# Kernel tuning notes

Measured on AMD Instinct MI355X. Metric: run time of the kernel, lower is better.

The kernel has to match this reference:

```python
import jax, jax.numpy as jnp
import numpy as np

WINDOW = 21
PATCH = 1
H_PARAM = 0.1
EPS = 1e-10


def _box_sum(x, w):
    # Sum over a w x w sliding window (VALID), per (batch, channel).
    return jax.lax.reduce_window(x, 0.0, jax.lax.add,
                                 (1, 1, w, w), (1, 1, 1, 1), 'VALID')


def setup_inputs() -> dict:
    key = jax.random.key(0)
    noisy = jax.random.uniform(key, (8, 3, 512, 512), dtype=jnp.float32)
    return {"noisy": noisy}


def reference(noisy) -> jnp.ndarray:
    # Faithful vectorization of the per-pixel loop for patch_size=1.
    # For each pixel p=(i,j):
    #   window = padded[i:i+W, j:j+W]; center = noisy[i,j]
    #   dists  = mean((window - center)^2)
    #   weights = exp(-dists / h^2)            # shape (B, C)
    #   patch  = window[0, 0] = padded[i, j]   # top-left of window (half_patch=0)
    #   out[:, c, i, j] = sum_b weights[b,c] * patch[b,c]   (sum over BATCH)
    #   wsum[:, c, i, j] = sum_b weights[b,c]
    # out = clamp(out / (wsum + 1e-10), 0, 1)
    h2 = H_PARAM * H_PARAM
    W = WINDOW
    pad = W // 2
    B, C, Hh, Ww = noisy.shape
    padded = jnp.pad(noisy, ((0, 0), (0, 0), (pad, pad), (pad, pad)), mode='reflect')

    # mean((window - center)^2) = (S2 - 2*center*S1 + W^2*center^2) / W^2
    s1 = _box_sum(padded, W)                  # (B, C, H, W)
    s2 = _box_sum(padded * padded, W)
    n_win = jnp.asarray(W * W, dtype=noisy.dtype)
    dists = (s2 - 2.0 * noisy * s1 + n_win * noisy * noisy) / n_win

    weights = jnp.exp(-dists / h2)            # (B, C, H, W)
    patch = padded[:, :, :Hh, :Ww]            # top-left pixel of each window

    num = jnp.sum(weights * patch, axis=0, keepdims=True)   # (1, C, H, W)
    den = jnp.sum(weights, axis=0, keepdims=True)
    out = num / (den + EPS)
    out = jnp.broadcast_to(out, noisy.shape)  # loop assigns same row to all b
    return jnp.clip(out, 0.0, 1.0)
```

## Files before the change

### kernel.cpp

```cpp
#include <hip/hip_runtime.h>

#define B 8
#define CCH 3
#define HH 512
#define WW 512
#define WIN 21
#define PAD 10
#define TSX 32
#define TSY 16
#define PTX (TSX + 2*PAD)
#define PTY (TSY + 2*PAD)

__global__ __launch_bounds__(256) void nlm_fused_kernel(const float* __restrict__ noisy,
                                                        float* __restrict__ out) {
    __shared__ float  tile[PTY][PTX + 1];
    __shared__ float2 hs[PTY][TSX + 1];

    const int tid = threadIdx.x;
    const int tx  = tid & 31;
    const int ty0 = (tid >> 5) * 2;

    const int x0 = blockIdx.x * TSX;
    const int y0 = blockIdx.y * TSY;
    const int ch = blockIdx.z;

    float num[2] = {0.f, 0.f};
    float den[2] = {0.f, 0.f};

    for (int b = 0; b < B; ++b) {
        const float* src = noisy + (size_t)(b * CCH + ch) * (HH * WW);

        for (int idx = tid; idx < PTY * PTX; idx += 256) {
            int r = idx / PTX;
            int c = idx - r * PTX;
            int gy = y0 + r - PAD;
            gy = (gy < 0) ? -gy : ((gy >= HH) ? (2 * (HH - 1) - gy) : gy);
            int gx = x0 + c - PAD;
            gx = (gx < 0) ? -gx : ((gx >= WW) ? (2 * (WW - 1) - gx) : gx);
            tile[r][c] = src[gy * WW + gx];
        }
        __syncthreads();

        for (int u = tid; u < PTY * 8; u += 256) {
            int r   = u >> 3;
            int cx0 = (u & 7) * 4;
            float s1 = 0.f, s2 = 0.f;
            #pragma unroll
            for (int k = 0; k < WIN; ++k) {
                float v = tile[r][cx0 + k];
                s1 += v;
                s2 += v * v;
            }
            hs[r][cx0] = make_float2(s1, s2);
            #pragma unroll
            for (int j = 1; j < 4; ++j) {
                float vo = tile[r][cx0 + j - 1];
                float vn = tile[r][cx0 + j + WIN - 1];
                s1 += vn - vo;
                s2 += vn * vn - vo * vo;
                hs[r][cx0 + j] = make_float2(s1, s2);
            }
        }
        __syncthreads();

        float vs1 = 0.f, vs2 = 0.f;
        #pragma unroll
        for (int k = 0; k < WIN; ++k) {
            float2 h = hs[ty0 + k][tx];
            vs1 += h.x;
            vs2 += h.y;
        }
        #pragma unroll
        for (int i = 0; i < 2; ++i) {
            if (i > 0) {
                float2 hn = hs[ty0 + i + WIN - 1][tx];
                float2 ho = hs[ty0 + i - 1][tx];
                vs1 += hn.x - ho.x;
                vs2 += hn.y - ho.y;
            }
            float a = tile[ty0 + i + PAD][tx + PAD];
            float p = tile[ty0 + i][tx];
            float d = (vs2 - 2.f * a * vs1 + (float)(WIN * WIN) * a * a)
            float w = __expf(d * -100.0f);
            num[i] += w * p;
            den[i] += w;
        }
        __syncthreads();
    }

    #pragma unroll
    for (int i = 0; i < 2; ++i) {
        int y = y0 + ty0 + i;
        int x = x0 + tx;
        float v = num[i] / (den[i] + 1e-10f);
        v = v < 0.f ? 0.f : (v > 1.f ? 1.f : v);
        #pragma unroll
        for (int b = 0; b < B; ++b) {
            out[((size_t)(b * CCH + ch) * HH + y) * WW + x] = v;
        }
    }
}

extern "C" void kernel_launch(void* const* d_in, const int* in_sizes, int n_in,
                              void* d_out, int out_size, void* d_ws, size_t ws_size,
                              hipStream_t stream) {
    const float* noisy = (const float*)d_in[0];
    float* out = (float*)d_out;
    dim3 grid(WW / TSX, HH / TSY, CCH);
    nlm_fused_kernel<<<grid, dim3(256), 0, stream>>>(noisy, out);
}
```

Baseline: 109.0 us.

## Vectorize tile loads and transpose horizontal-sum buffer for float4 LDS reads

Global tile loads become float4 reads, with a scalar fallback only at reflect-padded edges. Each thread in the horizontal-sum pass now loads its 24 tile values into registers as float4s. The horizontal sums are stored transposed (column-major, padded row), so the vertical pass reads two float2 entries per float4 LDS access. This is meant to cut global and LDS instruction counts, at the cost of more registers and possible LDS bank conflicts from the transposed layout.

Measured after the change: 103.3 us. -5.2%, faster.

```diff
diff --git a/kernel.cpp b/kernel.cpp
--- a/kernel.cpp
+++ b/kernel.cpp
@@ -8,13 +8,15 @@
 #define PAD 10
 #define TSX 32
 #define TSY 16
-#define PTX (TSX + 2*PAD)
-#define PTY (TSY + 2*PAD)
+#define PTX 52
+#define PTY 36
+#define TROW 56
+#define HROW 38
 
 __global__ __launch_bounds__(256) void nlm_fused_kernel(const float* __restrict__ noisy,
                                                         float* __restrict__ out) {
-    __shared__ float  tile[PTY][PTX + 1];
-    __shared__ float2 hs[PTY][TSX + 1];
+    __shared__ float  tile[PTY][TROW];
+    __shared__ float2 hs_t[TSX][HROW];
 
     const int tid = threadIdx.x;
     const int tx  = tid & 31;
@@ -24,79 +26,99 @@
     const int y0 = blockIdx.y * TSY;
     const int ch = blockIdx.z;
 
-    float num[2] = {0.f, 0.f};
-    float den[2] = {0.f, 0.f};
+    float num0 = 0.f, num1 = 0.f, den0 = 0.f, den1 = 0.f;
 
     for (int b = 0; b < B; ++b) {
         const float* src = noisy + (size_t)(b * CCH + ch) * (HH * WW);
 
-        for (int idx = tid; idx < PTY * PTX; idx += 256) {
-            int r = idx / PTX;
-            int c = idx - r * PTX;
+        for (int s = tid; s < PTY * 13; s += 256) {
+            int r  = s / 13;
+            int c4 = s - r * 13;
             int gy = y0 + r - PAD;
             gy = (gy < 0) ? -gy : ((gy >= HH) ? (2 * (HH - 1) - gy) : gy);
-            int gx = x0 + c - PAD;
-            gx = (gx < 0) ? -gx : ((gx >= WW) ? (2 * (WW - 1) - gx) : gx);
-            tile[r][c] = src[gy * WW + gx];
+            int gxs = x0 + (c4 << 2) - PAD;
+            float4 v;
+            if (gxs >= 0 && gxs <= WW - 4) {
+                v = *(const float4*)(src + gy * WW + gxs);
+            } else {
+                float tmp[4];
+                #pragma unroll
+                for (int t = 0; t < 4; ++t) {
+                    int gx = gxs + t;
+                    gx = (gx < 0) ? -gx : ((gx >= WW) ? (2 * (WW - 1) - gx) : gx);
+                    tmp[t] = src[gy * WW + gx];
+                }
+                v = make_float4(tmp[0], tmp[1], tmp[2], tmp[3]);
+            }
+            *(float4*)&tile[r][c4 << 2] = v;
         }
         __syncthreads();
 
         for (int u = tid; u < PTY * 8; u += 256) {
             int r   = u >> 3;
-            int cx0 = (u & 7) * 4;
+            int cx0 = (u & 7) << 2;
+            float v[24];
+            #pragma unroll
+            for (int q = 0; q < 6; ++q)
+                *(float4*)&v[q * 4] = *(const float4*)&tile[r][cx0 + q * 4];
             float s1 = 0.f, s2 = 0.f;
             #pragma unroll
-            for (int k = 0; k < WIN; ++k) {
-                float v = tile[r][cx0 + k];
-                s1 += v;
-                s2 += v * v;
-            }
-            hs[r][cx0] = make_float2(s1, s2);
+            for (int k = 0; k < WIN; ++k) { s1 += v[k]; s2 += v[k] * v[k]; }
+            hs_t[cx0][r] = make_float2(s1, s2);
             #pragma unroll
             for (int j = 1; j < 4; ++j) {
-                float vo = tile[r][cx0 + j - 1];
-                float vn = tile[r][cx0 + j + WIN - 1];
+                float vo = v[j - 1], vn = v[j + WIN - 1];
                 s1 += vn - vo;
                 s2 += vn * vn - vo * vo;
-                hs[r][cx0 + j] = make_float2(s1, s2);
+                hs_t[cx0 + j][r] = make_float2(s1, s2);
             }
         }
         __syncthreads();
 
-        float vs1 = 0.f, vs2 = 0.f;
+        float4 q0 = *(const float4*)&hs_t[tx][ty0];
+        float vs1 = q0.x + q0.z, vs2 = q0.y + q0.w;
         #pragma unroll
-        for (int k = 0; k < WIN; ++k) {
-            float2 h = hs[ty0 + k][tx];
-            vs1 += h.x;
-            vs2 += h.y;
+        for (int k = 1; k < 10; ++k) {
+            float4 q = *(const float4*)&hs_t[tx][ty0 + 2 * k];
+            vs1 += q.x + q.z;
+            vs2 += q.y + q.w;
         }
-        #pragma unroll
-        for (int i = 0; i < 2; ++i) {
-            if (i > 0) {
-                float2 hn = hs[ty0 + i + WIN - 1][tx];
-                float2 ho = hs[ty0 + i - 1][tx];
-                vs1 += hn.x - ho.x;
-                vs2 += hn.y - ho.y;
-            }
-            float a = tile[ty0 + i + PAD][tx + PAD];
-            float p = tile[ty0 + i][tx];
-            float d = (vs2 - 2.f * a * vs1 + (float)(WIN * WIN) * a * a)
-            float w = __expf(d * -100.0f);
-            num[i] += w * p;
-            den[i] += w;
+        float4 q10 = *(const float4*)&hs_t[tx][ty0 + 20];
+        vs1 += q10.x;
+        vs2 += q10.y;
+        {
+            float a = tile[ty0 + PAD][tx + PAD];
+            float p = tile[ty0][tx];
+            float dd = vs2 - 2.f * a * vs1 + 441.f * a * a;
+            float w = __expf(dd * (-100.f / 441.f));
+            num0 += w * p;
+            den0 += w;
+        }
+        vs1 += q10.z - q0.x;
+        vs2 += q10.w - q0.y;
+        {
+            float a = tile[ty0 + 1 + PAD][tx + PAD];
+            float p = tile[ty0 + 1][tx];
+            float dd = vs2 - 2.f * a * vs1 + 441.f * a * a;
+            float w = __expf(dd * (-100.f / 441.f));
+            num1 += w * p;
+            den1 += w;
         }
         __syncthreads();
     }
 
-    #pragma unroll
-    for (int i = 0; i < 2; ++i) {
-        int y = y0 + ty0 + i;
+    {
+        int y = y0 + ty0;
         int x = x0 + tx;
-        float v = num[i] / (den[i] + 1e-10f);
-        v = v < 0.f ? 0.f : (v > 1.f ? 1.f : v);
+        float v0 = num0 / (den0 + 1e-10f);
+        v0 = v0 < 0.f ? 0.f : (v0 > 1.f ? 1.f : v0);
+        float v1 = num1 / (den1 + 1e-10f);
+        v1 = v1 < 0.f ? 0.f : (v1 > 1.f ? 1.f : v1);
         #pragma unroll
         for (int b = 0; b < B; ++b) {
-            out[((size_t)(b * CCH + ch) * HH + y) * WW + x] = v;
+            size_t base = ((size_t)(b * CCH + ch) * HH + y) * WW + x;
+            out[base] = v0;
+            out[base + WW] = v1;
         }
     }
 }
```

## Prefetch next batch tile into registers, enlarge tile, transpose horizontal sums

Applied to the files above, without the earlier changes.

Each thread now loads a float4 of the next batch's padded tile into registers while the current batch is processed, overlapping global loads with compute. Tile height doubles to 32 rows with 4 outputs per thread, which amortizes the halo. The horizontal sums are stored transposed so each thread reads its own column. Loads and the exp are vectorized and strength-reduced. The cost is higher register use and larger LDS per block, and a 16x32 grid of 3-channel blocks leaves fewer blocks per CU.

Measured after the change: 88.94 us. 1.23x faster.

```diff
diff --git a/kernel.cpp b/kernel.cpp
--- a/kernel.cpp
+++ b/kernel.cpp
@@ -7,97 +7,158 @@
 #define WIN 21
 #define PAD 10
 #define TSX 32
-#define TSY 16
-#define PTX (TSX + 2*PAD)
-#define PTY (TSY + 2*PAD)
+#define TSY 32
+#define PTY 52
+#define TROW 60
+#define HSH 53
+#define NSLOT 676
 
-__global__ __launch_bounds__(256) void nlm_fused_kernel(const float* __restrict__ noisy,
-                                                        float* __restrict__ out) {
-    __shared__ float  tile[PTY][PTX + 1];
-    __shared__ float2 hs[PTY][TSX + 1];
+__global__ __launch_bounds__(256, 3) void nlm_fused_kernel(const float* __restrict__ noisy,
+                                                           float* __restrict__ out) {
+    __shared__ float  tile[PTY][TROW];
+    __shared__ float2 hs_t[TSX][HSH];
 
     const int tid = threadIdx.x;
-    const int tx  = tid & 31;
-    const int ty0 = (tid >> 5) * 2;
-
     const int x0 = blockIdx.x * TSX;
     const int y0 = blockIdx.y * TSY;
     const int ch = blockIdx.z;
 
-    float num[2] = {0.f, 0.f};
-    float den[2] = {0.f, 0.f};
+    int   rowbase[3], gxs[3];
+    float* ldsp[3];
+    bool  valid[3], edge[3];
+    #pragma unroll
+    for (int k = 0; k < 3; ++k) {
+        int s = tid + 256 * k;
+        valid[k] = (s < NSLOT);
+        int ss = valid[k] ? s : 0;
+        int r  = ss / 13;
+        int c4 = ss - r * 13;
+        int gy = y0 + r - PAD;
+        gy = (gy < 0) ? -gy : ((gy >= HH) ? (2 * (HH - 1) - gy) : gy);
+        int gx = x0 + (c4 << 2) - PAD;
+        rowbase[k] = gy * WW;
+        gxs[k]     = gx;
+        edge[k]    = (gx < 0) || (gx > WW - 4);
+        ldsp[k]    = &tile[r][c4 << 2];
+    }
+
+    const float* src0 = noisy + (size_t)ch * (HH * WW);
+    float4 pre[3];
+    #pragma unroll
+    for (int k = 0; k < 3; ++k) {
+        if (valid[k]) {
+            if (!edge[k]) {
+                pre[k] = *(const float4*)(src0 + rowbase[k] + gxs[k]);
+            } else {
+                float tmp[4];
+                #pragma unroll
+                for (int t = 0; t < 4; ++t) {
+                    int gx = gxs[k] + t;
+                    gx = (gx < 0) ? -gx : ((gx >= WW) ? (2 * (WW - 1) - gx) : gx);
+                    tmp[t] = src0[rowbase[k] + gx];
+                }
+                pre[k] = make_float4(tmp[0], tmp[1], tmp[2], tmp[3]);
+            }
+        }
+    }
+
+    float num[4] = {0.f, 0.f, 0.f, 0.f};
+    float den[4] = {0.f, 0.f, 0.f, 0.f};
+
+    const int tx  = tid & 31;
+    const int ty0 = (tid >> 5) << 2;
 
     for (int b = 0; b < B; ++b) {
-        const float* src = noisy + (size_t)(b * CCH + ch) * (HH * WW);
-
-        for (int idx = tid; idx < PTY * PTX; idx += 256) {
-            int r = idx / PTX;
-            int c = idx - r * PTX;
-            int gy = y0 + r - PAD;
-            gy = (gy < 0) ? -gy : ((gy >= HH) ? (2 * (HH - 1) - gy) : gy);
-            int gx = x0 + c - PAD;
-            gx = (gx < 0) ? -gx : ((gx >= WW) ? (2 * (WW - 1) - gx) : gx);
-            tile[r][c] = src[gy * WW + gx];
-        }
+        __syncthreads();
+        #pragma unroll
+        for (int k = 0; k < 3; ++k)
+            if (valid[k]) *(float4*)ldsp[k] = pre[k];
         __syncthreads();
 
-        for (int u = tid; u < PTY * 8; u += 256) {
-            int r   = u >> 3;
-            int cx0 = (u & 7) * 4;
+        if (b < B - 1) {
+            const float* srcn = noisy + (size_t)((b + 1) * CCH + ch) * (HH * WW);
+            #pragma unroll
+            for (int k = 0; k < 3; ++k) {
+                if (valid[k]) {
+                    if (!edge[k]) {
+                        pre[k] = *(const float4*)(srcn + rowbase[k] + gxs[k]);
+                    } else {
+                        float tmp[4];
+                        #pragma unroll
+                        for (int t = 0; t < 4; ++t) {
+                            int gx = gxs[k] + t;
+                            gx = (gx < 0) ? -gx : ((gx >= WW) ? (2 * (WW - 1) - gx) : gx);
+                            tmp[t] = srcn[rowbase[k] + gx];
+                        }
+                        pre[k] = make_float4(tmp[0], tmp[1], tmp[2], tmp[3]);
+                    }
+                }
+            }
+        }
+
+        if (tid < PTY * 4) {
+            int r   = tid >> 2;
+            int cx0 = (tid & 3) << 3;
+            float v[28];
+            #pragma unroll
+            for (int q = 0; q < 7; ++q)
+                *(float4*)&v[q * 4] = *(const float4*)&tile[r][cx0 + (q << 2)];
             float s1 = 0.f, s2 = 0.f;
             #pragma unroll
-            for (int k = 0; k < WIN; ++k) {
-                float v = tile[r][cx0 + k];
-                s1 += v;
-                s2 += v * v;
-            }
-            hs[r][cx0] = make_float2(s1, s2);
+            for (int k = 0; k <= 20; ++k) { s1 += v[k]; s2 = fmaf(v[k], v[k], s2); }
+            hs_t[cx0][r] = make_float2(s1, s2);
             #pragma unroll
-            for (int j = 1; j < 4; ++j) {
-                float vo = tile[r][cx0 + j - 1];
-                float vn = tile[r][cx0 + j + WIN - 1];
+            for (int j = 1; j < 8; ++j) {
+                float vo = v[j - 1], vn = v[j + 20];
                 s1 += vn - vo;
                 s2 += vn * vn - vo * vo;
-                hs[r][cx0 + j] = make_float2(s1, s2);
+                hs_t[cx0 + j][r] = make_float2(s1, s2);
             }
         }
         __syncthreads();
 
-        float vs1 = 0.f, vs2 = 0.f;
+        float2 h0 = hs_t[tx][ty0];
+        float2 h1 = hs_t[tx][ty0 + 1];
+        float2 h2 = hs_t[tx][ty0 + 2];
+        float vs1 = h0.x + h1.x + h2.x;
+        float vs2 = h0.y + h1.y + h2.y;
         #pragma unroll
-        for (int k = 0; k < WIN; ++k) {
-            float2 h = hs[ty0 + k][tx];
+        for (int k = 3; k <= 20; ++k) {
+            float2 h = hs_t[tx][ty0 + k];
             vs1 += h.x;
             vs2 += h.y;
         }
+        const float kE = (-100.0f / 441.0f) * 1.44269504088896f;
+        {
+            float a = tile[ty0 + PAD][tx + PAD];
+            float p = tile[ty0][tx];
+            float dd = fmaf(a, fmaf(441.f, a, -2.f * vs1), vs2);
+            float w = exp2f(dd * kE);
+            num[0] += w * p; den[0] += w;
+        }
         #pragma unroll
-        for (int i = 0; i < 2; ++i) {
-            if (i > 0) {
-                float2 hn = hs[ty0 + i + WIN - 1][tx];
-                float2 ho = hs[ty0 + i - 1][tx];
-                vs1 += hn.x - ho.x;
-                vs2 += hn.y - ho.y;
-            }
+        for (int i = 1; i < 4; ++i) {
+            float2 hn = hs_t[tx][ty0 + 20 + i];
+            float2 ho = (i == 1) ? h0 : ((i == 2) ? h1 : h2);
+            vs1 += hn.x - ho.x;
+            vs2 += hn.y - ho.y;
             float a = tile[ty0 + i + PAD][tx + PAD];
             float p = tile[ty0 + i][tx];
-            float d = (vs2 - 2.f * a * vs1 + (float)(WIN * WIN) * a * a)
-            float w = __expf(d * -100.0f);
-            num[i] += w * p;
-            den[i] += w;
+            float dd = fmaf(a, fmaf(441.f, a, -2.f * vs1), vs2);
+            float w = exp2f(dd * kE);
+            num[i] += w * p; den[i] += w;
         }
-        __syncthreads();
     }
 
     #pragma unroll
-    for (int i = 0; i < 2; ++i) {
+    for (int i = 0; i < 4; ++i) {
         int y = y0 + ty0 + i;
         int x = x0 + tx;
         float v = num[i] / (den[i] + 1e-10f);
         v = v < 0.f ? 0.f : (v > 1.f ? 1.f : v);
         #pragma unroll
-        for (int b = 0; b < B; ++b) {
+        for (int b = 0; b < B; ++b)
             out[((size_t)(b * CCH + ch) * HH + y) * WW + x] = v;
-        }
     }
 }
 
```
